# Performance work log

Hardware: AMD Instinct MI355X
Metric: run time of the kernel (lower is better)

Reference implementation:

```python
import jax, jax.numpy as jnp
import numpy as np

LMAX = 3
NDEG = LMAX + 1            # degrees l = 0..3
MDIM = 2 * LMAX + 1        # padded m dimension (7)
K = 128                    # channels per degree
N = 4096                   # number of samples (atomic environments)
NITER = 2                  # number_of_iterations

# CG paths (l1, l2) -> L with |l1-l2| <= L <= min(l1+l2, LMAX); 34 paths
PATHS = [(l1, l2, L)
         for L in range(NDEG)
         for l1 in range(NDEG)
         for l2 in range(NDEG)
         if abs(l1 - l2) <= L <= l1 + l2]


def setup_inputs() -> dict:
    key = jax.random.key(0)
    k1, k2, k3, k4 = jax.random.split(key, 4)

    # zero-mask padded m components: valid m < 2l+1 per degree l
    mmask = (jnp.arange(MDIM)[None, :] < (2 * jnp.arange(NDEG) + 1)[:, None])
    mmask = mmask.astype(jnp.float32)                      # [NDEG, MDIM]

    feats = jax.random.normal(k1, (NDEG, N, MDIM, K), dtype=jnp.float32)
    feats = feats * mmask[:, None, :, None]

    # CG-like coefficients, zero-padded per path to [2l1+1, 2l2+1, 2L+1]
    umask = np.zeros((len(PATHS), MDIM, MDIM, MDIM), dtype=np.float32)
    for p, (l1, l2, L) in enumerate(PATHS):
        umask[p, :2 * l1 + 1, :2 * l2 + 1, :2 * L + 1] = 1.0
    U = jax.random.normal(k2, (len(PATHS), MDIM, MDIM, MDIM), dtype=jnp.float32)
    U = 0.1 * U * jnp.asarray(umask)

    scale = 1.0 / np.sqrt(K)
    mixer_W = scale * jax.random.normal(k3, (NITER + 1, NDEG, K, K), dtype=jnp.float32)
    iter_W = scale * jax.random.normal(k4, (NITER, NDEG, K, K), dtype=jnp.float32)

    return {"feats": feats, "U": U, "mixer_W": mixer_W, "iter_W": iter_W}


def spherical_linear(f, W):
    # per-degree channel mix: f [NDEG, N, MDIM, K], W [NDEG, K, K]
    return jnp.einsum('lnmk,lkj->lnmj', f, W)


def tensor_product(f1, f2, U):
    # channel-wise CG tensor product, summed over paths into each output degree L
    out = jnp.zeros_like(f1)
    for p, (l1, l2, L) in enumerate(PATHS):
        out = out.at[L].add(jnp.einsum('nak,nbk,abc->nck', f1[l1], f2[l2], U[p]))
    return out


def reference(feats, U, mixer_W, iter_W):
    # mixed_densities = [mixer(density) for mixer in self.mixers]
    mixed = [spherical_linear(feats, mixer_W[i]) for i in range(NITER + 1)]
    cur = mixed[0]
    # CG iterations: residual( linear( tensor_product(cur, mixed[t+1]) ) )
    for t in range(NITER):
        tp = tensor_product(cur, mixed[t + 1], U)
        cur = cur + spherical_linear(tp, iter_W[t])
    return cur
```

## Files before the change

### kernel.cpp

```cpp
#include <hip/hip_runtime.h>

#define NSAMP 4096
#define KCH   128
#define MDIM  7

typedef __attribute__((ext_vector_type(8))) short bf16x8;
typedef __attribute__((ext_vector_type(4))) float f32x4;
typedef __attribute__((ext_vector_type(4))) unsigned u32x4;

static constexpr int RB[4] = {0, 1, 4, 9};
static constexpr int RE[4] = {1, 4, 9, 16};
static constexpr int PR_L[16] = {0,1,1,1,2,2,2,2,2,3,3,3,3,3,3,3};
static constexpr int PR_M[16] = {0,0,1,2,0,1,2,3,4,0,1,2,3,4,5,6};

static constexpr int PIDX[4][4][4] = {
  { { 0,-1,-1,-1},{-1, 1,-1,-1},{-1,-1, 2,-1},{-1,-1,-1, 3} },
  { {-1, 4,-1,-1},{ 5, 6, 7,-1},{-1, 8, 9,10},{-1,-1,11,12} },
  { {-1,-1,13,-1},{-1,14,15,16},{17,18,19,20},{-1,21,22,23} },
  { {-1,-1,-1,24},{-1,-1,25,26},{-1,27,28,29},{30,31,32,33} }
};

static constexpr int ZL[12] = {0,0,0,0,0,0, 1,1,1,1, 2,2};
static constexpr int ZM[12] = {1,2,3,4,5,6, 3,4,5,6, 5,6};

#define WP_BYTES 1310720u
#define BG_BYTES 16384u

static __device__ __forceinline__ unsigned short f2bf(float x) {
    unsigned u = __builtin_bit_cast(unsigned, x);
    u = u + 0x7FFFu + ((u >> 16) & 1u);
    return (unsigned short)(u >> 16);
}
static __device__ __forceinline__ float bf2f(unsigned short h) {
    unsigned u = ((unsigned)h) << 16;
    return __builtin_bit_cast(float, u);
}

__global__ __launch_bounds__(256) void cg_prep(const float* __restrict__ mW,
                                               const float* __restrict__ iW,
                                               unsigned short* __restrict__ Wp)
{
    int gid = blockIdx.x * 256 + threadIdx.x;
    int lane = gid & 63;
    int set  = gid >> 6;
    int spl = set & 1;
    int ks  = (set >> 1) & 3;
    int ct  = (set >> 3) & 7;
    int l   = (set >> 6) & 3;
    int mi  = set >> 8;
    const float* src = (mi < 3) ? (mW + ((size_t)mi * 4 + l) * (KCH * KCH))
                                : (iW + ((size_t)(mi - 3) * 4 + l) * (KCH * KCH));
    int j  = ct * 16 + (lane & 15);
    int kb = ks * 32 + (lane >> 4) * 8;
    unsigned short o[8];
#pragma unroll
    for (int e = 0; e < 8; ++e) {
        float w = src[(size_t)(kb + e) * KCH + j];
        unsigned short h = f2bf(w);
        o[e] = spl ? f2bf(w - bf2f(h)) : h;
    }
    uint4 pk;
    unsigned* pw = (unsigned*)&pk;
#pragma unroll
    for (int q = 0; q < 4; ++q) pw[q] = (unsigned)o[2*q] | ((unsigned)o[2*q+1] << 16);
    *(uint4*)(Wp + (size_t)set * 512 + lane * 8) = pk;
}

__global__ __launch_bounds__(256) void cg_prepg(const float* __restrict__ U,
                                                unsigned short* __restrict__ Bg)
{
    const int gid  = blockIdx.x * 256 + threadIdx.x;
    const int s    = gid >> 7;
    const int spl  = (gid >> 6) & 1;
    const int lane = gid & 63;
    const int c    = lane & 15;
    const int kb   = s * 32 + (lane >> 4) * 8;
    const int Lo   = PR_L[c], cm = PR_M[c];
    unsigned short o[8];
#pragma unroll
    for (int e = 0; e < 8; ++e) {
        const int k  = kb + e;
        const int i  = k >> 4, j = k & 15;
        const int l1 = PR_L[i], a = PR_M[i];
        const int l2 = PR_L[j], b = PR_M[j];
        const int p  = PIDX[Lo][l1][l2];
        float val = (p >= 0) ? U[p * 343 + (a * 7 + b) * 7 + cm] : 0.0f;
        unsigned short h = f2bf(val);
        o[e] = spl ? f2bf(val - bf2f(h)) : h;
    }
    uint4 pk;
    unsigned* pw = (unsigned*)&pk;
#pragma unroll
    for (int q = 0; q < 4; ++q) pw[q] = (unsigned)o[2*q] | ((unsigned)o[2*q+1] << 16);
    *(uint4*)(Bg + (size_t)((s * 2 + spl) * 64 + lane) * 8) = pk;
}

static __device__ __forceinline__ bf16x8 ldF(const unsigned short* P, int row16, int key, int c) {
    int cs = c ^ (key & 7);
    return *(const bf16x8*)(P + row16 * 128 + cs * 8);
}

static __device__ __forceinline__ void stage_feats1(const float* __restrict__ feats,
                                                    unsigned short* Fh, int tid, int n0)
{
    const int row = tid >> 1;
    const int r   = row >> 4;
    const int nlr = row & 15;
    const int kh  = tid & 1;
    const int l = PR_L[r], m = PR_M[r];
    const float* g = feats + (((size_t)l * NSAMP + (n0 + nlr)) * MDIM + m) * KCH + kh * 64;
    unsigned short* fh = Fh + row * 128;
#pragma unroll
    for (int c8 = 0; c8 < 8; ++c8) {
        f32x4 a = *(const f32x4*)(g + c8 * 8);
        f32x4 b = *(const f32x4*)(g + c8 * 8 + 4);
        float v[8] = {a[0], a[1], a[2], a[3], b[0], b[1], b[2], b[3]};
        uint4 ph;
        unsigned* pw = (unsigned*)&ph;
#pragma unroll
        for (int q = 0; q < 4; ++q)
            pw[q] = (unsigned)f2bf(v[2*q]) | ((unsigned)f2bf(v[2*q+1]) << 16);
        const int cs = (kh * 8 + c8) ^ (nlr & 7);
        *(uint4*)(fh + cs * 8) = ph;
    }
}

static __device__ __forceinline__ void mix_sweep1(const unsigned short* Fh,
                                                  const bf16x8* __restrict__ Wp, int mi,
                                                  int ct, int lane, f32x4 (&acc)[16])
{
    const int kg = lane >> 4;
    const int l15 = lane & 15;
#pragma unroll
    for (int r = 0; r < 16; ++r) { acc[r][0]=acc[r][1]=acc[r][2]=acc[r][3]=0.0f; }
#pragma unroll
    for (int ks = 0; ks < 4; ++ks) {
#pragma unroll
        for (int l = 0; l < 4; ++l) {
            const int s0 = (((mi * 4 + l) * 8 + ct) * 4 + ks) * 2;
            bf16x8 bh = Wp[(size_t)s0 * 64 + lane];
            bf16x8 bl = Wp[(size_t)(s0 + 1) * 64 + lane];
#pragma unroll
            for (int r = RB[l]; r < RE[l]; ++r) {
                bf16x8 ah = ldF(Fh, r * 16 + l15, l15, ks * 4 + kg);
                acc[r] = __builtin_amdgcn_mfma_f32_16x16x32_bf16(ah, bh, acc[r], 0, 0, 0);
                acc[r] = __builtin_amdgcn_mfma_f32_16x16x32_bf16(ah, bl, acc[r], 0, 0, 0);
            }
        }
    }
}

static __device__ __forceinline__ void acc_to_lds(const f32x4 (&acc)[16], unsigned short* P,
                                                  int ct, int lane)
{
    const int kg = lane >> 4;
    const int l15 = lane & 15;
    const int chnk = ct * 2 + (l15 >> 3);
#pragma unroll
    for (int r = 0; r < 16; ++r) {
#pragma unroll
        for (int q = 0; q < 4; ++q) {
            const int smp = kg * 4 + q;
            const int cs = chnk ^ (smp & 7);
            P[(smp * 16 + r) * 128 + cs * 8 + (l15 & 7)] = f2bf(acc[r][q]);
        }
    }
}

static __device__ __forceinline__ void tp_iter(unsigned short* Ch, const unsigned short* Mt,
                                               const bf16x8* __restrict__ Bg,
                                               const bf16x8* __restrict__ Wp, int miW,
                                               int ct, int lane, f32x4 (&racc)[16])
{
    const int kg  = lane >> 4;
    const int l15 = lane & 15;
    const int i0 = kg >> 1;
    const int j0 = (kg & 1) * 8;
    const int chnk = ct * 2 + (l15 >> 3);
    const int chA  = ct * 2 + (kg >> 1);
    const int co4  = (kg * 4) & 7;

    bf16x8 bgh[8], bgl[8];
#pragma unroll
    for (int s = 0; s < 8; ++s) {
        bgh[s] = Bg[(size_t)(s * 2 + 0) * 64 + lane];
        bgl[s] = Bg[(size_t)(s * 2 + 1) * 64 + lane];
    }

    f32x4 tpa[4];
#pragma unroll 1
    for (int g = 0; g < 4; ++g) {
#pragma unroll
        for (int uu = 0; uu < 4; ++uu) {
            const int u = g * 4 + uu;
            const int cs = chnk ^ (u & 7);
            const unsigned short* cb = Ch + u * 2048 + cs * 8 + (l15 & 7);
            const unsigned short* mb = Mt + u * 2048 + cs * 8 + (l15 & 7);
            float cvv[8], mvv[8];
#pragma unroll
            for (int s = 0; s < 8; ++s) cvv[s] = bf2f(cb[(i0 + 2 * s) * 128]);
#pragma unroll
            for (int e = 0; e < 8; ++e) mvv[e] = bf2f(mb[(j0 + e) * 128]);
            f32x4 acc = {0.0f, 0.0f, 0.0f, 0.0f};
#pragma unroll
            for (int s = 0; s < 8; ++s) {
                float pf[8];
#pragma unroll
                for (int e = 0; e < 8; ++e) pf[e] = cvv[s] * mvv[e];
                unsigned ah[4];
#pragma unroll
                for (int d = 0; d < 4; ++d) {
                    asm("v_cvt_pk_bf16_f32 %0, %1, %2" : "=v"(ah[d]) : "v"(pf[2*d]), "v"(pf[2*d+1]));
                }
                const u32x4 AH = {ah[0], ah[1], ah[2], ah[3]};
                const bf16x8 a_h = __builtin_bit_cast(bf16x8, AH);
                acc = __builtin_amdgcn_mfma_f32_16x16x32_bf16(a_h, bgh[s], acc, 0, 0, 0);
                acc = __builtin_amdgcn_mfma_f32_16x16x32_bf16(a_h, bgl[s], acc, 0, 0, 0);
            }
            tpa[uu] = acc;
        }
        __syncthreads();
#pragma unroll
        for (int uu = 0; uu < 4; ++uu) {
            const int u = g * 4 + uu;
            const int cs = chA ^ ((u ^ l15) & 7);
            const int soff = (u * 16 + l15) * 128 + cs * 8 + co4;
            const unsigned short h0 = f2bf(tpa[uu][0]);
            const unsigned short h1 = f2bf(tpa[uu][1]);
            const unsigned short h2 = f2bf(tpa[uu][2]);
            const unsigned short h3 = f2bf(tpa[uu][3]);
            *(unsigned*)(Ch + soff)     = (unsigned)h0 | ((unsigned)h1 << 16);
            *(unsigned*)(Ch + soff + 2) = (unsigned)h2 | ((unsigned)h3 << 16);
        }
    }
    __syncthreads();

#pragma unroll
    for (int ks = 0; ks < 4; ++ks) {
#pragma unroll
        for (int l = 0; l < 4; ++l) {
            const int s0 = (((miW * 4 + l) * 8 + ct) * 4 + ks) * 2;
            bf16x8 bh = Wp[(size_t)s0 * 64 + lane];
            bf16x8 bl = Wp[(size_t)(s0 + 1) * 64 + lane];
#pragma unroll
            for (int r = RB[l]; r < RE[l]; ++r) {
                bf16x8 ah = ldF(Ch, l15 * 16 + r, l15 ^ r, ks * 4 + kg);
                racc[r] = __builtin_amdgcn_mfma_f32_16x16x32_bf16(ah, bh, racc[r], 0, 0, 0);
                racc[r] = __builtin_amdgcn_mfma_f32_16x16x32_bf16(ah, bl, racc[r], 0, 0, 0);
            }
        }
    }
}

__global__ __launch_bounds__(512, 2) void cg_fuseA(const float* __restrict__ feats,
                                                   const bf16x8* __restrict__ Wp,
                                                   const bf16x8* __restrict__ Bg,
                                                   unsigned short* __restrict__ Pcur,
                                                   int base)
{
    extern __shared__ char smem[];
    unsigned short* Fh = (unsigned short*)smem;
    unsigned short* Tp = Fh + 32768;

    const int tid  = threadIdx.x;
    const int lane = tid & 63;
    const int ct   = tid >> 6;
    const int nl0  = blockIdx.x * 16;
    const int kg   = lane >> 4;
    const int l15  = lane & 15;
    const int j    = ct * 16 + l15;

    stage_feats1(feats, Fh, tid, base + nl0);
    __syncthreads();

    f32x4 accC[16], accM[16];
    mix_sweep1(Fh, Wp, 0, ct, lane, accC);
    mix_sweep1(Fh, Wp, 1, ct, lane, accM);
    __syncthreads();

    acc_to_lds(accC, Fh, ct, lane);
    acc_to_lds(accM, Tp, ct, lane);
    __syncthreads();

    tp_iter(Fh, Tp, Bg, Wp, 3, ct, lane, accC);

#pragma unroll
    for (int r = 0; r < 16; ++r) {
#pragma unroll
        for (int q = 0; q < 4; ++q) {
            const int nl = nl0 + kg * 4 + q;
            Pcur[((size_t)nl * 16 + r) * KCH + j] = f2bf(accC[r][q]);
        }
    }
}

__global__ __launch_bounds__(512, 2) void cg_fuseB(const float* __restrict__ feats,
                                                   const bf16x8* __restrict__ Wp,
                                                   const bf16x8* __restrict__ Bg,
                                                   const unsigned short* __restrict__ Pcur,
                                                   float* __restrict__ gout,
                                                   int base)
{
    extern __shared__ char smem[];
    unsigned short* Fh = (unsigned short*)smem;
    unsigned short* Tp = Fh + 32768;

    const int tid  = threadIdx.x;
    const int lane = tid & 63;
    const int ct   = tid >> 6;
    const int nl0  = blockIdx.x * 16;
    const int kg   = lane >> 4;
    const int l15  = lane & 15;
    const int j    = ct * 16 + l15;

    f32x4 racc[16];
#pragma unroll
    for (int r = 0; r < 16; ++r) {
#pragma unroll
        for (int q = 0; q < 4; ++q) {
            const int nl = nl0 + kg * 4 + q;
            racc[r][q] = bf2f(Pcur[((size_t)nl * 16 + r) * KCH + j]);
        }
    }

    stage_feats1(feats, Fh, tid, base + nl0);
    __syncthreads();

    f32x4 accM[16];
    mix_sweep1(Fh, Wp, 2, ct, lane, accM);
    __syncthreads();

    acc_to_lds(racc, Fh, ct, lane);
    acc_to_lds(accM, Tp, ct, lane);
    __syncthreads();

    tp_iter(Fh, Tp, Bg, Wp, 4, ct, lane, racc);

#pragma unroll
    for (int r = 0; r < 16; ++r) {
#pragma unroll
        for (int q = 0; q < 4; ++q) {
            const int n = base + nl0 + kg * 4 + q;
            gout[(((size_t)PR_L[r] * NSAMP + n) * MDIM + PR_M[r]) * KCH + j] = racc[r][q];
        }
    }
    {
        const int j2 = tid & 127;
        const int g  = tid >> 7;
#pragma unroll
        for (int z = 0; z < 12; ++z) {
#pragma unroll
            for (int i = 0; i < 4; ++i) {
                const int n = base + nl0 + g * 4 + i;
                gout[(((size_t)ZL[z] * NSAMP + n) * MDIM + ZM[z]) * KCH + j2] = 0.0f;
            }
        }
    }
}

extern "C" void kernel_launch(void* const* d_in, const int* in_sizes, int n_in,
                              void* d_out, int out_size, void* d_ws, size_t ws_size,
                              hipStream_t stream)
{
    const float* feats = (const float*)d_in[0];
    const float* U     = (const float*)d_in[1];
    const float* mW    = (const float*)d_in[2];
    const float* iW    = (const float*)d_in[3];
    float* out = (float*)d_out;

    const size_t fixed = (size_t)WP_BYTES + BG_BYTES;
    size_t avail = (ws_size > fixed) ? (ws_size - fixed) : 0;
    int NC = (int)(avail / 4096);
    NC = (NC / 16) * 16;
    if (NC > NSAMP) NC = NSAMP;
    if (NC < 16) return;

    char* wsb = (char*)d_ws;
    unsigned short* Wp   = (unsigned short*)wsb;
    unsigned short* Bg   = (unsigned short*)(wsb + WP_BYTES);
    unsigned short* Pcur = (unsigned short*)(wsb + fixed);

    hipFuncSetAttribute(reinterpret_cast<const void*>(cg_fuseA),
                        hipFuncAttributeMaxDynamicSharedMemorySize, 131072);
    hipFuncSetAttribute(reinterpret_cast<const void*>(cg_fuseB),
                        hipFuncAttributeMaxDynamicSharedMemorySize, 131072);

    cg_prep<<<320, 256, 0, stream>>>(mW, iW, Wp);
    cg_prepg<<<4, 256, 0, stream>>>(U, Bg);

    for (int base = 0; base < NSAMP; base += NC) {
        const int nc = (NSAMP - base < NC) ? (NSAMP - base) : NC;
        cg_fuseA<<<nc / 16, 512, 131072, stream>>>(feats, (const bf16x8*)Wp,
                                                   (const bf16x8*)Bg, Pcur, base);
        cg_fuseB<<<nc / 16, 512, 131072, stream>>>(feats, (const bf16x8*)Wp,
                                                   (const bf16x8*)Bg, Pcur, out, base);
    }
}
```

Baseline: 95.39 us.

## Split fused CG kernels across two 512-thread wave groups in 1024-thread blocks

Doubles the block to 1024 threads (16 waves) and splits the work between two wave groups. In kernel A each group computes one mixer projection. In both kernels the tensor-product passes over the 16 m-rows are divided so each group handles 8, and the final iter linear runs only in group 0. The Bg fragments are now loaded from global inside the inner loop rather than held in registers. The aim is more waves per block for better latency hiding and shorter per-wave serial work. The cost is an idle group during the iter sweep, extra barriers, and occupancy of one block per CU given 128KB LDS.

Result: slower. 118.0 us (+23.7%).

```diff
diff --git a/kernel.cpp b/kernel.cpp
--- a/kernel.cpp
+++ b/kernel.cpp
@@ -100,18 +100,19 @@
     return *(const bf16x8*)(P + row16 * 128 + cs * 8);
 }
 
-static __device__ __forceinline__ void stage_feats1(const float* __restrict__ feats,
-                                                    unsigned short* Fh, int tid, int n0)
-{
-    const int row = tid >> 1;
+static __device__ __forceinline__ void stage_feats1024(const float* __restrict__ feats,
+                                                       unsigned short* Fh, int tid, int n0)
+{
+    const int row = tid >> 2;
     const int r   = row >> 4;
     const int nlr = row & 15;
-    const int kh  = tid & 1;
+    const int q4  = tid & 3;
     const int l = PR_L[r], m = PR_M[r];
-    const float* g = feats + (((size_t)l * NSAMP + (n0 + nlr)) * MDIM + m) * KCH + kh * 64;
+    const float* g = feats + (((size_t)l * NSAMP + (n0 + nlr)) * MDIM + m) * KCH;
     unsigned short* fh = Fh + row * 128;
 #pragma unroll
-    for (int c8 = 0; c8 < 8; ++c8) {
+    for (int i = 0; i < 4; ++i) {
+        const int c8 = q4 * 4 + i;
         f32x4 a = *(const f32x4*)(g + c8 * 8);
         f32x4 b = *(const f32x4*)(g + c8 * 8 + 4);
         float v[8] = {a[0], a[1], a[2], a[3], b[0], b[1], b[2], b[3]};
@@ -120,7 +121,7 @@
 #pragma unroll
         for (int q = 0; q < 4; ++q)
             pw[q] = (unsigned)f2bf(v[2*q]) | ((unsigned)f2bf(v[2*q+1]) << 16);
-        const int cs = (kh * 8 + c8) ^ (nlr & 7);
+        const int cs = c8 ^ (nlr & 7);
         *(uint4*)(fh + cs * 8) = ph;
     }
 }
@@ -167,74 +168,75 @@
     }
 }
 
-static __device__ __forceinline__ void tp_iter(unsigned short* Ch, const unsigned short* Mt,
+static __device__ __forceinline__ void tp_pass(const unsigned short* Ch, const unsigned short* Mt,
                                                const bf16x8* __restrict__ Bg,
-                                               const bf16x8* __restrict__ Wp, int miW,
-                                               int ct, int lane, f32x4 (&racc)[16])
+                                               int u0, int ct, int lane, f32x4 (&tpa)[4])
 {
     const int kg  = lane >> 4;
     const int l15 = lane & 15;
     const int i0 = kg >> 1;
     const int j0 = (kg & 1) * 8;
     const int chnk = ct * 2 + (l15 >> 3);
-    const int chA  = ct * 2 + (kg >> 1);
-    const int co4  = (kg * 4) & 7;
-
-    bf16x8 bgh[8], bgl[8];
-#pragma unroll
-    for (int s = 0; s < 8; ++s) {
-        bgh[s] = Bg[(size_t)(s * 2 + 0) * 64 + lane];
-        bgl[s] = Bg[(size_t)(s * 2 + 1) * 64 + lane];
-    }
-
-    f32x4 tpa[4];
-#pragma unroll 1
-    for (int g = 0; g < 4; ++g) {
-#pragma unroll
-        for (int uu = 0; uu < 4; ++uu) {
-            const int u = g * 4 + uu;
-            const int cs = chnk ^ (u & 7);
-            const unsigned short* cb = Ch + u * 2048 + cs * 8 + (l15 & 7);
-            const unsigned short* mb = Mt + u * 2048 + cs * 8 + (l15 & 7);
-            float cvv[8], mvv[8];
-#pragma unroll
-            for (int s = 0; s < 8; ++s) cvv[s] = bf2f(cb[(i0 + 2 * s) * 128]);
-#pragma unroll
-            for (int e = 0; e < 8; ++e) mvv[e] = bf2f(mb[(j0 + e) * 128]);
-            f32x4 acc = {0.0f, 0.0f, 0.0f, 0.0f};
-#pragma unroll
-            for (int s = 0; s < 8; ++s) {
-                float pf[8];
-#pragma unroll
-                for (int e = 0; e < 8; ++e) pf[e] = cvv[s] * mvv[e];
-                unsigned ah[4];
-#pragma unroll
-                for (int d = 0; d < 4; ++d) {
-                    asm("v_cvt_pk_bf16_f32 %0, %1, %2" : "=v"(ah[d]) : "v"(pf[2*d]), "v"(pf[2*d+1]));
-                }
-                const u32x4 AH = {ah[0], ah[1], ah[2], ah[3]};
-                const bf16x8 a_h = __builtin_bit_cast(bf16x8, AH);
-                acc = __builtin_amdgcn_mfma_f32_16x16x32_bf16(a_h, bgh[s], acc, 0, 0, 0);
-                acc = __builtin_amdgcn_mfma_f32_16x16x32_bf16(a_h, bgl[s], acc, 0, 0, 0);
-            }
-            tpa[uu] = acc;
-        }
-        __syncthreads();
-#pragma unroll
-        for (int uu = 0; uu < 4; ++uu) {
-            const int u = g * 4 + uu;
-            const int cs = chA ^ ((u ^ l15) & 7);
-            const int soff = (u * 16 + l15) * 128 + cs * 8 + co4;
-            const unsigned short h0 = f2bf(tpa[uu][0]);
-            const unsigned short h1 = f2bf(tpa[uu][1]);
-            const unsigned short h2 = f2bf(tpa[uu][2]);
-            const unsigned short h3 = f2bf(tpa[uu][3]);
-            *(unsigned*)(Ch + soff)     = (unsigned)h0 | ((unsigned)h1 << 16);
-            *(unsigned*)(Ch + soff + 2) = (unsigned)h2 | ((unsigned)h3 << 16);
-        }
-    }
-    __syncthreads();
-
+#pragma unroll
+    for (int uu = 0; uu < 4; ++uu) {
+        const int u = u0 + uu;
+        const int cs = chnk ^ (u & 7);
+        const unsigned short* cb = Ch + u * 2048 + cs * 8 + (l15 & 7);
+        const unsigned short* mb = Mt + u * 2048 + cs * 8 + (l15 & 7);
+        float cvv[8], mvv[8];
+#pragma unroll
+        for (int s = 0; s < 8; ++s) cvv[s] = bf2f(cb[(i0 + 2 * s) * 128]);
+#pragma unroll
+        for (int e = 0; e < 8; ++e) mvv[e] = bf2f(mb[(j0 + e) * 128]);
+        f32x4 acc = {0.0f, 0.0f, 0.0f, 0.0f};
+#pragma unroll
+        for (int s = 0; s < 8; ++s) {
+            float pf[8];
+#pragma unroll
+            for (int e = 0; e < 8; ++e) pf[e] = cvv[s] * mvv[e];
+            unsigned ah[4];
+#pragma unroll
+            for (int d = 0; d < 4; ++d) {
+                asm("v_cvt_pk_bf16_f32 %0, %1, %2" : "=v"(ah[d]) : "v"(pf[2*d]), "v"(pf[2*d+1]));
+            }
+            const u32x4 AH = {ah[0], ah[1], ah[2], ah[3]};
+            const bf16x8 a_h = __builtin_bit_cast(bf16x8, AH);
+            const bf16x8 bh = Bg[(size_t)(s * 2 + 0) * 64 + lane];
+            const bf16x8 bl = Bg[(size_t)(s * 2 + 1) * 64 + lane];
+            acc = __builtin_amdgcn_mfma_f32_16x16x32_bf16(a_h, bh, acc, 0, 0, 0);
+            acc = __builtin_amdgcn_mfma_f32_16x16x32_bf16(a_h, bl, acc, 0, 0, 0);
+        }
+        tpa[uu] = acc;
+    }
+}
+
+static __device__ __forceinline__ void tp_write(unsigned short* Ch, int u0, int ct, int lane,
+                                                const f32x4 (&tpa)[4])
+{
+    const int kg  = lane >> 4;
+    const int l15 = lane & 15;
+    const int chA = ct * 2 + (kg >> 1);
+    const int co4 = (kg * 4) & 7;
+#pragma unroll
+    for (int uu = 0; uu < 4; ++uu) {
+        const int u = u0 + uu;
+        const int cs = chA ^ ((u ^ l15) & 7);
+        const int soff = (u * 16 + l15) * 128 + cs * 8 + co4;
+        const unsigned short h0 = f2bf(tpa[uu][0]);
+        const unsigned short h1 = f2bf(tpa[uu][1]);
+        const unsigned short h2 = f2bf(tpa[uu][2]);
+        const unsigned short h3 = f2bf(tpa[uu][3]);
+        *(unsigned*)(Ch + soff)     = (unsigned)h0 | ((unsigned)h1 << 16);
+        *(unsigned*)(Ch + soff + 2) = (unsigned)h2 | ((unsigned)h3 << 16);
+    }
+}
+
+static __device__ __forceinline__ void iter_sweep(const unsigned short* Tp,
+                                                  const bf16x8* __restrict__ Wp, int miW,
+                                                  int ct, int lane, f32x4 (&racc)[16])
+{
+    const int kg = lane >> 4;
+    const int l15 = lane & 15;
 #pragma unroll
     for (int ks = 0; ks < 4; ++ks) {
 #pragma unroll
@@ -244,7 +246,7 @@
             bf16x8 bl = Wp[(size_t)(s0 + 1) * 64 + lane];
 #pragma unroll
             for (int r = RB[l]; r < RE[l]; ++r) {
-                bf16x8 ah = ldF(Ch, l15 * 16 + r, l15 ^ r, ks * 4 + kg);
+                bf16x8 ah = ldF(Tp, l15 * 16 + r, l15 ^ r, ks * 4 + kg);
                 racc[r] = __builtin_amdgcn_mfma_f32_16x16x32_bf16(ah, bh, racc[r], 0, 0, 0);
                 racc[r] = __builtin_amdgcn_mfma_f32_16x16x32_bf16(ah, bl, racc[r], 0, 0, 0);
             }
@@ -252,11 +254,11 @@
     }
 }
 
-__global__ __launch_bounds__(512, 2) void cg_fuseA(const float* __restrict__ feats,
-                                                   const bf16x8* __restrict__ Wp,
-                                                   const bf16x8* __restrict__ Bg,
-                                                   unsigned short* __restrict__ Pcur,
-                                                   int base)
+__global__ __launch_bounds__(1024, 1) void cg_fuseA(const float* __restrict__ feats,
+                                                    const bf16x8* __restrict__ Wp,
+                                                    const bf16x8* __restrict__ Bg,
+                                                    unsigned short* __restrict__ Pcur,
+                                                    int base)
 {
     extern __shared__ char smem[];
     unsigned short* Fh = (unsigned short*)smem;
@@ -264,42 +266,53 @@
 
     const int tid  = threadIdx.x;
     const int lane = tid & 63;
-    const int ct   = tid >> 6;
+    const int wid  = tid >> 6;
+    const int grp  = wid >> 3;
+    const int ct   = wid & 7;
     const int nl0  = blockIdx.x * 16;
     const int kg   = lane >> 4;
     const int l15  = lane & 15;
     const int j    = ct * 16 + l15;
 
-    stage_feats1(feats, Fh, tid, base + nl0);
-    __syncthreads();
-
-    f32x4 accC[16], accM[16];
-    mix_sweep1(Fh, Wp, 0, ct, lane, accC);
-    mix_sweep1(Fh, Wp, 1, ct, lane, accM);
-    __syncthreads();
-
-    acc_to_lds(accC, Fh, ct, lane);
-    acc_to_lds(accM, Tp, ct, lane);
-    __syncthreads();
-
-    tp_iter(Fh, Tp, Bg, Wp, 3, ct, lane, accC);
-
-#pragma unroll
-    for (int r = 0; r < 16; ++r) {
-#pragma unroll
-        for (int q = 0; q < 4; ++q) {
-            const int nl = nl0 + kg * 4 + q;
-            Pcur[((size_t)nl * 16 + r) * KCH + j] = f2bf(accC[r][q]);
-        }
-    }
-}
-
-__global__ __launch_bounds__(512, 2) void cg_fuseB(const float* __restrict__ feats,
-                                                   const bf16x8* __restrict__ Wp,
-                                                   const bf16x8* __restrict__ Bg,
-                                                   const unsigned short* __restrict__ Pcur,
-                                                   float* __restrict__ gout,
-                                                   int base)
+    stage_feats1024(feats, Fh, tid, base + nl0);
+    __syncthreads();
+
+    f32x4 acc[16];
+    mix_sweep1(Fh, Wp, grp, ct, lane, acc);
+    __syncthreads();
+
+    acc_to_lds(acc, grp == 0 ? Fh : Tp, ct, lane);
+    __syncthreads();
+
+    f32x4 tpa[4];
+    const int ub = grp * 8;
+    tp_pass(Fh, Tp, Bg, ub, ct, lane, tpa);
+    __syncthreads();
+    tp_write(Fh, ub, ct, lane, tpa);
+    tp_pass(Fh, Tp, Bg, ub + 4, ct, lane, tpa);
+    __syncthreads();
+    tp_write(Fh, ub + 4, ct, lane, tpa);
+    __syncthreads();
+
+    if (grp == 0) {
+        iter_sweep(Fh, Wp, 3, ct, lane, acc);
+#pragma unroll
+        for (int r = 0; r < 16; ++r) {
+#pragma unroll
+            for (int q = 0; q < 4; ++q) {
+                const int nl = nl0 + kg * 4 + q;
+                Pcur[((size_t)nl * 16 + r) * KCH + j] = f2bf(acc[r][q]);
+            }
+        }
+    }
+}
+
+__global__ __launch_bounds__(1024, 1) void cg_fuseB(const float* __restrict__ feats,
+                                                    const bf16x8* __restrict__ Wp,
+                                                    const bf16x8* __restrict__ Bg,
+                                                    const unsigned short* __restrict__ Pcur,
+                                                    float* __restrict__ gout,
+                                                    int base)
 {
     extern __shared__ char smem[];
     unsigned short* Fh = (unsigned short*)smem;
@@ -307,51 +320,65 @@
 
     const int tid  = threadIdx.x;
     const int lane = tid & 63;
-    const int ct   = tid >> 6;
+    const int wid  = tid >> 6;
+    const int grp  = wid >> 3;
+    const int ct   = wid & 7;
     const int nl0  = blockIdx.x * 16;
     const int kg   = lane >> 4;
     const int l15  = lane & 15;
     const int j    = ct * 16 + l15;
 
-    f32x4 racc[16];
-#pragma unroll
-    for (int r = 0; r < 16; ++r) {
-#pragma unroll
-        for (int q = 0; q < 4; ++q) {
-            const int nl = nl0 + kg * 4 + q;
-            racc[r][q] = bf2f(Pcur[((size_t)nl * 16 + r) * KCH + j]);
-        }
-    }
-
-    stage_feats1(feats, Fh, tid, base + nl0);
-    __syncthreads();
-
-    f32x4 accM[16];
-    mix_sweep1(Fh, Wp, 2, ct, lane, accM);
-    __syncthreads();
-
-    acc_to_lds(racc, Fh, ct, lane);
-    acc_to_lds(accM, Tp, ct, lane);
-    __syncthreads();
-
-    tp_iter(Fh, Tp, Bg, Wp, 4, ct, lane, racc);
-
-#pragma unroll
-    for (int r = 0; r < 16; ++r) {
-#pragma unroll
-        for (int q = 0; q < 4; ++q) {
-            const int n = base + nl0 + kg * 4 + q;
-            gout[(((size_t)PR_L[r] * NSAMP + n) * MDIM + PR_M[r]) * KCH + j] = racc[r][q];
-        }
-    }
+    f32x4 acc[16];
+    if (grp == 0) {
+#pragma unroll
+        for (int r = 0; r < 16; ++r) {
+#pragma unroll
+            for (int q = 0; q < 4; ++q) {
+                const int nl = nl0 + kg * 4 + q;
+                acc[r][q] = bf2f(Pcur[((size_t)nl * 16 + r) * KCH + j]);
+            }
+        }
+    }
+
+    stage_feats1024(feats, Fh, tid, base + nl0);
+    __syncthreads();
+
+    if (grp == 1) mix_sweep1(Fh, Wp, 2, ct, lane, acc);
+    __syncthreads();
+
+    acc_to_lds(acc, grp == 0 ? Fh : Tp, ct, lane);
+    __syncthreads();
+
+    f32x4 tpa[4];
+    const int ub = grp * 8;
+    tp_pass(Fh, Tp, Bg, ub, ct, lane, tpa);
+    __syncthreads();
+    tp_write(Fh, ub, ct, lane, tpa);
+    tp_pass(Fh, Tp, Bg, ub + 4, ct, lane, tpa);
+    __syncthreads();
+    tp_write(Fh, ub + 4, ct, lane, tpa);
+    __syncthreads();
+
+    if (grp == 0) {
+        iter_sweep(Fh, Wp, 4, ct, lane, acc);
+#pragma unroll
+        for (int r = 0; r < 16; ++r) {
+#pragma unroll
+            for (int q = 0; q < 4; ++q) {
+                const int n = base + nl0 + kg * 4 + q;
+                gout[(((size_t)PR_L[r] * NSAMP + n) * MDIM + PR_M[r]) * KCH + j] = acc[r][q];
+            }
+        }
+    }
+
     {
         const int j2 = tid & 127;
         const int g  = tid >> 7;
 #pragma unroll
         for (int z = 0; z < 12; ++z) {
 #pragma unroll
-            for (int i = 0; i < 4; ++i) {
-                const int n = base + nl0 + g * 4 + i;
+            for (int i = 0; i < 2; ++i) {
+                const int n = base + nl0 + g * 2 + i;
                 gout[(((size_t)ZL[z] * NSAMP + n) * MDIM + ZM[z]) * KCH + j2] = 0.0f;
             }
         }
@@ -390,9 +417,9 @@
 
     for (int base = 0; base < NSAMP; base += NC) {
         const int nc = (NSAMP - base < NC) ? (NSAMP - base) : NC;
-        cg_fuseA<<<nc / 16, 512, 131072, stream>>>(feats, (const bf16x8*)Wp,
-                                                   (const bf16x8*)Bg, Pcur, base);
-        cg_fuseB<<<nc / 16, 512, 131072, stream>>>(feats, (const bf16x8*)Wp,
-                                                   (const bf16x8*)Bg, Pcur, out, base);
-    }
-}
+        cg_fuseA<<<nc / 16, 1024, 131072, stream>>>(feats, (const bf16x8*)Wp,
+                                                    (const bf16x8*)Bg, Pcur, base);
+        cg_fuseB<<<nc / 16, 1024, 131072, stream>>>(feats, (const bf16x8*)Wp,
+                                                    (const bf16x8*)Bg, Pcur, out, base);
+    }
+}
```
